# Kernel optimization log

Measured on AMD Instinct MI355X. Metric: run time of the kernel, lower is better.

The kernel has to match this reference:

```python
import jax, jax.numpy as jnp
import numpy as np

BS = 8192
INPUT_DIM = 4096
LAYER_DIMS = [64, 256, 64]
BLOCK_DIM = LAYER_DIMS[0]
N_BLOCKS = INPUT_DIM // BLOCK_DIM


def setup_inputs() -> dict:
    key = jax.random.key(0)
    kx, kw1, kw2 = jax.random.split(key, 3)
    x = jax.random.normal(kx, (BS, INPUT_DIM), dtype=jnp.float32)
    # BlockLinear params: weight ~ randn, bias ~ zeros (as in torch source)
    W1 = jax.random.normal(kw1, (N_BLOCKS, LAYER_DIMS[0], LAYER_DIMS[1]), dtype=jnp.float32)
    b1 = jnp.zeros((N_BLOCKS, 1, LAYER_DIMS[1]), dtype=jnp.float32)
    W2 = jax.random.normal(kw2, (N_BLOCKS, LAYER_DIMS[1], LAYER_DIMS[2]), dtype=jnp.float32)
    b2 = jnp.zeros((N_BLOCKS, 1, LAYER_DIMS[2]), dtype=jnp.float32)
    return {"x": x, "W1": W1, "b1": b1, "W2": W2, "b2": b2}


def reference(x, W1, b1, W2, b2):
    bs = x.shape[0]
    # [bs, input_dim] -> [n_blocks, bs, block_dim]
    h = x.reshape(bs, N_BLOCKS, BLOCK_DIM).transpose(1, 0, 2)
    # BlockLinear 1 (bmm + bias) then exact GELU (torch nn.GELU default)
    h = jnp.einsum('nbi,nio->nbo', h, W1) + b1
    h = jax.nn.gelu(h, approximate=False)
    # BlockLinear 2
    h = jnp.einsum('nbi,nio->nbo', h, W2) + b2
    # [n_blocks, bs, out_block] -> [bs, n_blocks*out_block]
    return h.transpose(1, 0, 2).reshape(bs, -1)
```

## Files before the change

### kernel.cpp

```cpp
#include <hip/hip_runtime.h>

using f16x8 = _Float16 __attribute__((ext_vector_type(8)));
using f32x4 = float __attribute__((ext_vector_type(4)));

#define BS      8192
#define IN_DIM  4096
#define NB      64
#define BD      64
#define HID     256
#define OD      64
#define GY      32

__device__ __forceinline__ float gelu_f(float z) {
    float t = z * z;
    float p = __builtin_fmaf(0.044715f * z, t, z);
    float e = __builtin_amdgcn_exp2f(p * 2.3021193f);
    float r = __builtin_amdgcn_rcpf(e + 1.0f);
    return __builtin_fmaf(-z, r, z);
}

__global__ __launch_bounds__(256) void prep_weights(
    const float* __restrict__ w1g, const float* __restrict__ w2g,
    f16x8* __restrict__ ws1, f16x8* __restrict__ ws2) {
    const int n = blockIdx.x;
    const int t = threadIdx.x;
    const float* W1n = w1g + (size_t)n * (BD * HID);
    const float* W2n = w2g + (size_t)n * (HID * OD);
    #pragma unroll
    for (int it = 0; it < 8; ++it) {
        int e = it * 256 + t;
        {
            int ht = e >> 7, ks = (e >> 6) & 1, le = e & 63;
            int ge = le >> 4, oo = le & 15;
            f16x8 v;
            #pragma unroll
            for (int j = 0; j < 8; ++j)
                v[j] = (_Float16)W1n[(size_t)(ks * 32 + ge * 8 + j) * HID + ht * 16 + oo];
            ws1[(size_t)n * 2048 + e] = v;
        }
        {
            int p = e >> 8, n2 = (e >> 6) & 3, le = e & 63;
            int ge = le >> 4, ce = le & 15;
            f16x8 v;
            #pragma unroll
            for (int j = 0; j < 8; ++j)
                v[j] = (_Float16)W2n[(size_t)(p * 32 + ((j >> 2) << 4) + ge * 4 + (j & 3)) * OD + n2 * 16 + ce];
            ws2[(size_t)n * 2048 + e] = v;
        }
    }
}

__global__ __launch_bounds__(512, 4) void blockmlp_kernel(
    const float* __restrict__ xg,
    const f16x8* __restrict__ ws1, const f16x8* __restrict__ ws2,
    const float* __restrict__ b1g, const float* __restrict__ b2g,
    float* __restrict__ outg) {

    __shared__ f16x8 W1F[2048];
    __shared__ f16x8 W2L[2048];
    __shared__ float b1L[HID];

    const int tid = threadIdx.x;
    const int w   = tid >> 6;
    const int l   = tid & 63;
    const int g   = l >> 4;
    const int l15 = l & 15;
    const int n   = blockIdx.x;

    const f16x8* p1 = ws1 + (size_t)n * 2048;
    const f16x8* p2 = ws2 + (size_t)n * 2048;
    f16x8 s1[4], s2[4];
    #pragma unroll
    for (int it = 0; it < 4; ++it) { s1[it] = p1[it * 512 + tid]; }
    #pragma unroll
    for (int it = 0; it < 4; ++it) { s2[it] = p2[it * 512 + tid]; }
    #pragma unroll
    for (int it = 0; it < 4; ++it) { W1F[it * 512 + tid] = s1[it]; }
    #pragma unroll
    for (int it = 0; it < 4; ++it) { W2L[it * 512 + tid] = s2[it]; }

    if (tid < HID) b1L[tid] = b1g[n * HID + tid];

    float b2b[4];
    #pragma unroll
    for (int n2 = 0; n2 < 4; ++n2) b2b[n2] = b2g[n * OD + n2 * 16 + l15];

    __syncthreads();

    const int row0 = blockIdx.y * 256 + w * 32;

    f16x8 xa[2][2];
    #pragma unroll
    for (int rs = 0; rs < 2; ++rs)
        #pragma unroll
        for (int ks = 0; ks < 2; ++ks) {
            const float* px = xg + (size_t)(row0 + rs * 16 + l15) * IN_DIM + n * BD + ks * 32 + g * 8;
            float4 lo = *(const float4*)px;
            float4 hi = *(const float4*)(px + 4);
            f16x8 v;
            v[0] = (_Float16)lo.x; v[1] = (_Float16)lo.y;
            v[2] = (_Float16)lo.z; v[3] = (_Float16)lo.w;
            v[4] = (_Float16)hi.x; v[5] = (_Float16)hi.y;
            v[6] = (_Float16)hi.z; v[7] = (_Float16)hi.w;
            xa[rs][ks] = v;
        }

    const f32x4 z4 = {0.0f, 0.0f, 0.0f, 0.0f};
    f32x4 c2[2][4];
    #pragma unroll
    for (int rs = 0; rs < 2; ++rs)
        #pragma unroll
        for (int n2 = 0; n2 < 4; ++n2) c2[rs][n2] = z4;

    #pragma unroll
    for (int p = 0; p < 8; ++p) {
        f32x4 c1[2][2];
        #pragma unroll
        for (int htl = 0; htl < 2; ++htl) {
            f32x4 ca = z4, cb = z4;
            #pragma unroll
            for (int ks = 0; ks < 2; ++ks) {
                f16x8 wf = W1F[(((p * 2 + htl) * 2) + ks) * 64 + l];
                ca = __builtin_amdgcn_mfma_f32_16x16x32_f16(wf, xa[0][ks], ca, 0, 0, 0);
                cb = __builtin_amdgcn_mfma_f32_16x16x32_f16(wf, xa[1][ks], cb, 0, 0, 0);
            }
            c1[htl][0] = ca; c1[htl][1] = cb;
        }
        f32x4 b1a = *(const f32x4*)&b1L[(p * 2 + 0) * 16 + g * 4];
        f32x4 b1b = *(const f32x4*)&b1L[(p * 2 + 1) * 16 + g * 4];
        f16x8 a2[2];
        #pragma unroll
        for (int rs = 0; rs < 2; ++rs) {
            f16x8 v;
            #pragma unroll
            for (int q = 0; q < 4; ++q) {
                v[q]     = (_Float16)gelu_f(c1[0][rs][q] + b1a[q]);
                v[q + 4] = (_Float16)gelu_f(c1[1][rs][q] + b1b[q]);
            }
            a2[rs] = v;
        }
        #pragma unroll
        for (int n2 = 0; n2 < 4; ++n2) {
            f16x8 bf = W2L[(p * 4 + n2) * 64 + l];
            c2[0][n2] = __builtin_amdgcn_mfma_f32_16x16x32_f16(a2[0], bf, c2[0][n2], 0, 0, 0);
            c2[1][n2] = __builtin_amdgcn_mfma_f32_16x16x32_f16(a2[1], bf, c2[1][n2], 0, 0, 0);
        }
    }

    #pragma unroll
    for (int rs = 0; rs < 2; ++rs)
        #pragma unroll
        for (int n2 = 0; n2 < 4; ++n2)
            #pragma unroll
            for (int q = 0; q < 4; ++q) {
                int row = row0 + rs * 16 + g * 4 + q;
                outg[(size_t)row * IN_DIM + n * BD + n2 * 16 + l15] = c2[rs][n2][q] + b2b[n2];
            }
}

extern "C" void kernel_launch(void* const* d_in, const int* in_sizes, int n_in,
                              void* d_out, int out_size, void* d_ws, size_t ws_size,
                              hipStream_t stream) {
    const float* x  = (const float*)d_in[0];
    const float* W1 = (const float*)d_in[1];
    const float* b1 = (const float*)d_in[2];
    const float* W2 = (const float*)d_in[3];
    const float* b2 = (const float*)d_in[4];
    float* out = (float*)d_out;

    f16x8* ws1 = (f16x8*)d_ws;
    f16x8* ws2 = ws1 + (size_t)NB * 2048;

    hipLaunchKernelGGL(prep_weights, dim3(NB), dim3(256), 0, stream, W1, W2, ws1, ws2);
    hipLaunchKernelGGL(blockmlp_kernel, dim3(NB, GY), dim3(512), 0, stream,
                       x, ws1, ws2, b1, b2, out);
}
```

Before: 77.65 us.

## Loop over row slabs per block, fold biases into accumulators, use sigmoid GELU

```diff
diff --git a/kernel.cpp b/kernel.cpp
--- a/kernel.cpp
+++ b/kernel.cpp
@@ -9,14 +9,13 @@
 #define BD      64
 #define HID     256
 #define OD      64
-#define GY      32
+#define GYP     8
+#define SLABS   4
 
 __device__ __forceinline__ float gelu_f(float z) {
-    float t = z * z;
-    float p = __builtin_fmaf(0.044715f * z, t, z);
-    float e = __builtin_amdgcn_exp2f(p * 2.3021193f);
+    float e = __builtin_amdgcn_exp2f(z * -2.4554443f);
     float r = __builtin_amdgcn_rcpf(e + 1.0f);
-    return __builtin_fmaf(-z, r, z);
+    return z * r;
 }
 
 __global__ __launch_bounds__(256) void prep_weights(
@@ -87,75 +86,82 @@
 
     __syncthreads();
 
-    const int row0 = blockIdx.y * 256 + w * 32;
+    const int base = blockIdx.y * (SLABS * 256) + w * 32;
 
-    f16x8 xa[2][2];
     #pragma unroll
-    for (int rs = 0; rs < 2; ++rs)
+    for (int s = 0; s < SLABS; ++s) {
+        const int row0 = base + s * 256;
+
+        f16x8 xa[2][2];
         #pragma unroll
-        for (int ks = 0; ks < 2; ++ks) {
-            const float* px = xg + (size_t)(row0 + rs * 16 + l15) * IN_DIM + n * BD + ks * 32 + g * 8;
-            float4 lo = *(const float4*)px;
-            float4 hi = *(const float4*)(px + 4);
-            f16x8 v;
-            v[0] = (_Float16)lo.x; v[1] = (_Float16)lo.y;
-            v[2] = (_Float16)lo.z; v[3] = (_Float16)lo.w;
-            v[4] = (_Float16)hi.x; v[5] = (_Float16)hi.y;
-            v[6] = (_Float16)hi.z; v[7] = (_Float16)hi.w;
-            xa[rs][ks] = v;
+        for (int rs = 0; rs < 2; ++rs)
+            #pragma unroll
+            for (int ks = 0; ks < 2; ++ks) {
+                const float* px = xg + (size_t)(row0 + rs * 16 + l15) * IN_DIM + n * BD + ks * 32 + g * 8;
+                float4 lo = *(const float4*)px;
+                float4 hi = *(const float4*)(px + 4);
+                f16x8 v;
+                v[0] = (_Float16)lo.x; v[1] = (_Float16)lo.y;
+                v[2] = (_Float16)lo.z; v[3] = (_Float16)lo.w;
+                v[4] = (_Float16)hi.x; v[5] = (_Float16)hi.y;
+                v[6] = (_Float16)hi.z; v[7] = (_Float16)hi.w;
+                xa[rs][ks] = v;
+            }
+
+        f32x4 c2[2][4];
+        #pragma unroll
+        for (int rs = 0; rs < 2; ++rs)
+            #pragma unroll
+            for (int n2 = 0; n2 < 4; ++n2) {
+                f32x4 ci;
+                ci[0] = b2b[n2]; ci[1] = b2b[n2]; ci[2] = b2b[n2]; ci[3] = b2b[n2];
+                c2[rs][n2] = ci;
+            }
+
+        #pragma unroll
+        for (int p = 0; p < 8; ++p) {
+            f32x4 c1[2][2];
+            #pragma unroll
+            for (int htl = 0; htl < 2; ++htl) {
+                f32x4 ca = *(const f32x4*)&b1L[(p * 2 + htl) * 16 + g * 4];
+                f32x4 cb = ca;
+                #pragma unroll
+                for (int ks = 0; ks < 2; ++ks) {
+                    f16x8 wf = W1F[(((p * 2 + htl) * 2) + ks) * 64 + l];
+                    ca = __builtin_amdgcn_mfma_f32_16x16x32_f16(wf, xa[0][ks], ca, 0, 0, 0);
+                    cb = __builtin_amdgcn_mfma_f32_16x16x32_f16(wf, xa[1][ks], cb, 0, 0, 0);
+                }
+                c1[htl][0] = ca; c1[htl][1] = cb;
+            }
+            f16x8 a2[2];
+            #pragma unroll
+            for (int rs = 0; rs < 2; ++rs) {
+                f16x8 v;
+                #pragma unroll
+                for (int q = 0; q < 4; ++q) {
+                    v[q]     = (_Float16)gelu_f(c1[0][rs][q]);
+                    v[q + 4] = (_Float16)gelu_f(c1[1][rs][q]);
+                }
+                a2[rs] = v;
+            }
+            #pragma unroll
+            for (int n2 = 0; n2 < 4; ++n2) {
+                f16x8 bf = W2L[(p * 4 + n2) * 64 + l];
+                c2[0][n2] = __builtin_amdgcn_mfma_f32_16x16x32_f16(a2[0], bf, c2[0][n2], 0, 0, 0);
+                c2[1][n2] = __builtin_amdgcn_mfma_f32_16x16x32_f16(a2[1], bf, c2[1][n2], 0, 0, 0);
+            }
         }
 
-    const f32x4 z4 = {0.0f, 0.0f, 0.0f, 0.0f};
-    f32x4 c2[2][4];
-    #pragma unroll
-    for (int rs = 0; rs < 2; ++rs)
         #pragma unroll
-        for (int n2 = 0; n2 < 4; ++n2) c2[rs][n2] = z4;
-
-    #pragma unroll
-    for (int p = 0; p < 8; ++p) {
-        f32x4 c1[2][2];
-        #pragma unroll
-        for (int htl = 0; htl < 2; ++htl) {
-            f32x4 ca = z4, cb = z4;
+        for (int rs = 0; rs < 2; ++rs)
             #pragma unroll
-            for (int ks = 0; ks < 2; ++ks) {
-                f16x8 wf = W1F[(((p * 2 + htl) * 2) + ks) * 64 + l];
-                ca = __builtin_amdgcn_mfma_f32_16x16x32_f16(wf, xa[0][ks], ca, 0, 0, 0);
-                cb = __builtin_amdgcn_mfma_f32_16x16x32_f16(wf, xa[1][ks], cb, 0, 0, 0);
-            }
-            c1[htl][0] = ca; c1[htl][1] = cb;
-        }
-        f32x4 b1a = *(const f32x4*)&b1L[(p * 2 + 0) * 16 + g * 4];
-        f32x4 b1b = *(const f32x4*)&b1L[(p * 2 + 1) * 16 + g * 4];
-        f16x8 a2[2];
-        #pragma unroll
-        for (int rs = 0; rs < 2; ++rs) {
-            f16x8 v;
-            #pragma unroll
-            for (int q = 0; q < 4; ++q) {
-                v[q]     = (_Float16)gelu_f(c1[0][rs][q] + b1a[q]);
-                v[q + 4] = (_Float16)gelu_f(c1[1][rs][q] + b1b[q]);
-            }
-            a2[rs] = v;
-        }
-        #pragma unroll
-        for (int n2 = 0; n2 < 4; ++n2) {
-            f16x8 bf = W2L[(p * 4 + n2) * 64 + l];
-            c2[0][n2] = __builtin_amdgcn_mfma_f32_16x16x32_f16(a2[0], bf, c2[0][n2], 0, 0, 0);
-            c2[1][n2] = __builtin_amdgcn_mfma_f32_16x16x32_f16(a2[1], bf, c2[1][n2], 0, 0, 0);
-        }
+            for (int n2 = 0; n2 < 4; ++n2)
+                #pragma unroll
+                for (int q = 0; q < 4; ++q) {
+                    int row = row0 + rs * 16 + g * 4 + q;
+                    outg[(size_t)row * IN_DIM + n * BD + n2 * 16 + l15] = c2[rs][n2][q];
+                }
     }
-
-    #pragma unroll
-    for (int rs = 0; rs < 2; ++rs)
-        #pragma unroll
-        for (int n2 = 0; n2 < 4; ++n2)
-            #pragma unroll
-            for (int q = 0; q < 4; ++q) {
-                int row = row0 + rs * 16 + g * 4 + q;
-                outg[(size_t)row * IN_DIM + n * BD + n2 * 16 + l15] = c2[rs][n2][q] + b2b[n2];
-            }
 }
 
 extern "C" void kernel_launch(void* const* d_in, const int* in_sizes, int n_in,
@@ -172,6 +178,6 @@
     f16x8* ws2 = ws1 + (size_t)NB * 2048;
 
     hipLaunchKernelGGL(prep_weights, dim3(NB), dim3(256), 0, stream, W1, W2, ws1, ws2);
-    hipLaunchKernelGGL(blockmlp_kernel, dim3(NB, GY), dim3(512), 0, stream,
+    hipLaunchKernelGGL(blockmlp_kernel, dim3(NB, GYP), dim3(512), 0, stream,
                        x, ws1, ws2, b1, b2, out);
 }
```

Measured after the change: 78.90 us. No clear change (+1.6%).
